# Performance work log

Hardware: AMD Instinct MI355X
Metric: run time of the kernel (lower is better)

Reference implementation:

```python
import jax, jax.numpy as jnp
import numpy as np

B, N = 4, 2048
EMB, HID = 64, 256
LENGTHSCALES = (0.5, 1.0, 2.0, 4.0)
H = len(LENGTHSCALES)
HEAD = HID // H  # 64, divides evenly
LAYERS = 4
IN_DIM = 3 + EMB + 3
EPS_LN = 1e-5


def _layer_norm(x, g, b):
    mu = jnp.mean(x, axis=-1, keepdims=True)
    var = jnp.mean((x - mu) ** 2, axis=-1, keepdims=True)
    return (x - mu) * jax.lax.rsqrt(var + EPS_LN) * g + b


def setup_inputs() -> dict:
    key = jax.random.key(0)
    ks = iter(jax.random.split(key, 32))
    p = lambda shape, s=0.02: jax.random.normal(next(ks), shape, jnp.float32) * s
    inp = {
        "latent_vars": jax.random.normal(next(ks), (B, N, 3), jnp.float32),
        "x_coords": jax.random.normal(next(ks), (B, N, 3), jnp.float32),
        "atom_embeddings": jax.random.normal(next(ks), (B, N, EMB), jnp.float32),
        # input MLP
        "in_W": p((IN_DIM, HID)), "in_b": jnp.zeros((HID,), jnp.float32),
        # per-layer kernel attention: per-head value projections + output projection
        "val_W": p((LAYERS, H, HID, HEAD)), "val_b": jnp.zeros((LAYERS, H, HEAD), jnp.float32),
        "attn_W": p((LAYERS, H * HEAD, HID)), "attn_b": jnp.zeros((LAYERS, HID), jnp.float32),
        # layer norms
        "ln1_g": jnp.ones((LAYERS, HID), jnp.float32), "ln1_b": jnp.zeros((LAYERS, HID), jnp.float32),
        "ln2_g": jnp.ones((LAYERS, HID), jnp.float32), "ln2_b": jnp.zeros((LAYERS, HID), jnp.float32),
        # FFN (hidden -> 2*hidden -> hidden)
        "ffn_W1": p((LAYERS, HID, 2 * HID)), "ffn_b1": jnp.zeros((LAYERS, 2 * HID), jnp.float32),
        "ffn_W2": p((LAYERS, 2 * HID, HID)), "ffn_b2": jnp.zeros((LAYERS, HID), jnp.float32),
        # output MLP
        "out_W1": p((HID, HID)), "out_b1": jnp.zeros((HID,), jnp.float32),
        "out_W2": p((HID, 3)), "out_b2": jnp.zeros((3,), jnp.float32),
    }
    return inp


def _forward(latent_vars, x_coords, atom_embeddings, in_W, in_b, val_W, val_b,
             attn_W, attn_b, ln1_g, ln1_b, ln2_g, ln2_b,
             ffn_W1, ffn_b1, ffn_W2, ffn_b2, out_W1, out_b1, out_W2, out_b2):
    # input MLP
    x = jnp.concatenate([x_coords, atom_embeddings, latent_vars], axis=-1)  # [B,N,70]
    feats = jax.nn.relu(x @ in_W + in_b)  # [B,N,HID]

    # RBF attention weights depend only on coords + fixed lengthscales -> compute once
    diff = x_coords[:, :, None, :] - x_coords[:, None, :, :]  # [B,N,N,3]
    d2 = jnp.sum(diff * diff, axis=-1)  # [B,N,N]
    ls2 = jnp.asarray(LENGTHSCALES, jnp.float32) ** 2  # [H]
    A = jnp.exp(-d2[None, :, :, :] / ls2[:, None, None, None])  # [H,B,N,N]
    A = A / (jnp.sum(A, axis=-1, keepdims=True) + 1e-8)

    for l in range(LAYERS):
        V = jnp.einsum('bnf,hfd->bnhd', feats, val_W[l]) + val_b[l]  # [B,N,H,HEAD]
        att = jnp.einsum('hbij,bjhd->bihd', A, V)  # [B,N,H,HEAD]
        att = att.reshape(att.shape[0], att.shape[1], H * HEAD) @ attn_W[l] + attn_b[l]
        feats = _layer_norm(feats + att, ln1_g[l], ln1_b[l])
        h = jax.nn.relu(feats @ ffn_W1[l] + ffn_b1[l]) @ ffn_W2[l] + ffn_b2[l]
        feats = _layer_norm(feats + h, ln2_g[l], ln2_b[l])

    return jax.nn.relu(feats @ out_W1 + out_b1) @ out_W2 + out_b2  # [B,N,3]


def reference(latent_vars, x_coords, atom_embeddings, in_W, in_b, val_W, val_b,
              attn_W, attn_b, ln1_g, ln1_b, ln2_g, ln2_b,
              ffn_W1, ffn_b1, ffn_W2, ffn_b2, out_W1, out_b1, out_W2, out_b2):
    return _forward(latent_vars, x_coords, atom_embeddings, in_W, in_b, val_W, val_b,
                    attn_W, attn_b, ln1_g, ln1_b, ln2_g, ln2_b,
                    ffn_W1, ffn_b1, ffn_W2, ffn_b2, out_W1, out_b1, out_W2, out_b2)
```

## Files before the change

kernel.cpp:

```cpp
#include <hip/hip_runtime.h>

#define B_ 4
#define N_ 2048
#define R_ (B_ * N_)
#define HID_ 256
#define EMB_ 64
#define IN_DIM_ 70
#define H_ 4
#define HEAD_ 64
#define FFN_ 512
#define LAYERS_ 4

typedef __attribute__((ext_vector_type(8))) short short8;
typedef __attribute__((ext_vector_type(4))) float f32x4;
typedef unsigned short ushort;

static __device__ __forceinline__ ushort f2bf(float f) {
    unsigned u = __builtin_bit_cast(unsigned, f);
    u += 0x7fffu + ((u >> 16) & 1u);
    return (ushort)(u >> 16);
}
static __device__ __forceinline__ float bf2f(ushort u) {
    unsigned x = ((unsigned)u) << 16;
    return __builtin_bit_cast(float, x);
}

#define GLOAD_LDS16(g, l)                                              \
    __builtin_amdgcn_global_load_lds(                                  \
        (const __attribute__((address_space(1))) void*)(g),            \
        (__attribute__((address_space(3))) void*)(l), 16, 0, 0)

#define MFMA16(a, b, c) __builtin_amdgcn_mfma_f32_16x16x32_bf16(a, b, c, 0, 0, 0)

__global__ __launch_bounds__(256) void pack_weights(const float* __restrict__ valW,
                                                    const float* __restrict__ attnW,
                                                    const float* __restrict__ ffnW1,
                                                    const float* __restrict__ ffnW2,
                                                    const float* __restrict__ outW1,
                                                    ushort* __restrict__ wp) {
    int idx = blockIdx.x * 256 + threadIdx.x;
    float v;
    if (idx < 262144) {
        int l = idx >> 16, c = (idx >> 8) & 255, k = idx & 255;
        v = valW[((l * 4 + (c >> 6)) * 256 + k) * 64 + (c & 63)];
    } else if (idx < 524288) {
        int i2 = idx - 262144;
        int l = i2 >> 16, c = (i2 >> 8) & 255, k = i2 & 255;
        v = attnW[l * 65536 + k * 256 + c];
    } else if (idx < 1048576) {
        int i2 = idx - 524288;
        int l = i2 >> 17, c = (i2 >> 8) & 511, k = i2 & 255;
        v = ffnW1[l * 131072 + k * 512 + c];
    } else if (idx < 1572864) {
        int i2 = idx - 1048576;
        int l = i2 >> 17, c = (i2 >> 9) & 255, k = i2 & 511;
        v = ffnW2[l * 131072 + k * 256 + c];
    } else {
        int i2 = idx - 1572864;
        int c = i2 >> 8, k = i2 & 255;
        v = outW1[k * 256 + c];
    }
    wp[idx] = f2bf(v);
}

__global__ __launch_bounds__(256) void input_mlp(const float* __restrict__ xc,
                                                 const float* __restrict__ emb,
                                                 const float* __restrict__ lat,
                                                 const float* __restrict__ W,
                                                 const float* __restrict__ b,
                                                 float* __restrict__ feats,
                                                 ushort* __restrict__ featsb) {
    __shared__ float xr[8][IN_DIM_ + 2];
    int t = threadIdx.x;
    int row0 = blockIdx.x * 8;
    for (int idx = t; idx < 8 * IN_DIM_; idx += 256) {
        int r = idx / IN_DIM_, f = idx % IN_DIM_;
        int rr = row0 + r;
        float v;
        if (f < 3)       v = xc[rr * 3 + f];
        else if (f < 67) v = emb[rr * EMB_ + (f - 3)];
        else             v = lat[rr * 3 + (f - 67)];
        xr[r][f] = v;
    }
    __syncthreads();
    float acc[8] = {0.f, 0.f, 0.f, 0.f, 0.f, 0.f, 0.f, 0.f};
    for (int f = 0; f < IN_DIM_; ++f) {
        float w = W[f * HID_ + t];
#pragma unroll
        for (int r = 0; r < 8; ++r) acc[r] += xr[r][f] * w;
    }
    float bb = b[t];
#pragma unroll
    for (int r = 0; r < 8; ++r) {
        float v = fmaxf(acc[r] + bb, 0.f);
        feats[(row0 + r) * HID_ + t] = v;
        featsb[(row0 + r) * HID_ + t] = f2bf(v);
    }
}

__global__ __launch_bounds__(256) void ebuild(const float* __restrict__ xc,
                                              ushort* __restrict__ E) {
    __shared__ float4 civ[64];
    __shared__ float4 cjv[512];
    int t = threadIdx.x;
    int jb = blockIdx.x;
    int ibl = blockIdx.y;
    int b = blockIdx.z;
    const float* xb = xc + (size_t)b * N_ * 3;
    if (t < 64) {
        const float* p = &xb[(ibl * 64 + t) * 3];
        float x = p[0], y = p[1], z = p[2];
        civ[t] = make_float4(x, y, z, x * x + y * y + z * z);
    }
#pragma unroll
    for (int s = 0; s < 2; ++s) {
        int j = s * 256 + t;
        const float* p = &xb[(jb * 512 + j) * 3];
        float x = p[0], y = p[1], z = p[2];
        cjv[j] = make_float4(x, y, z, x * x + y * y + z * z);
    }
    __syncthreads();
    int lane = t & 63, ig = t >> 6;
    float4 cj[8];
#pragma unroll
    for (int e = 0; e < 8; ++e) cj[e] = cjv[lane * 8 + e];
    const float ch0 = -4.f * 1.44269504088896f;
    ushort* Ebase = E + ((size_t)b * 2048 + ibl * 64) * 2048 + (size_t)jb * 512 + lane * 8;

    for (int r = 0; r < 16; ++r) {
        int i = ig * 16 + r;
        float4 ci = civ[i];
        float d[8];
#pragma unroll
        for (int e = 0; e < 8; ++e)
            d[e] = (ci.w + cj[e].w) -
                   2.f * (ci.x * cj[e].x + ci.y * cj[e].y + ci.z * cj[e].z);
        float ch = ch0;
#pragma unroll
        for (int h = 0; h < 4; ++h) {
            float ex[8];
#pragma unroll
            for (int e = 0; e < 8; ++e) ex[e] = exp2f(d[e] * ch);
            union { unsigned u[4]; uint4 v; } pk;
#pragma unroll
            for (int q = 0; q < 4; ++q)
                asm("v_cvt_pk_bf16_f32 %0, %1, %2"
                    : "=v"(pk.u[q]) : "v"(ex[2 * q]), "v"(ex[2 * q + 1]));
            *(uint4*)(Ebase + (size_t)h * 4 * 2048 * 2048 + (size_t)i * 2048) = pk.v;
            ch *= 0.25f;
        }
    }
}

__global__ __launch_bounds__(256, 1) void pv_gemm(const ushort* __restrict__ E,
                                                  const ushort* __restrict__ Vt,
                                                  ushort* __restrict__ attb) {
    __shared__ __align__(16) char lds[98304];
    int t = threadIdx.x;
    int l = t & 63, w = t >> 6;
    int lr = l & 15, g = l >> 4;

    int f = blockIdx.x;
    int xcd = f & 7, s = f >> 3;
    int combo = xcd * 2 + (s >> 4);
    int ib = s & 15;
    int b = combo & 3, h = combo >> 2;
    int i_base = ib * 128;
    int hc = h * 64;

    const ushort* Eb = E + (size_t)(h * 4 + b) * 2048 * 2048;

    const ushort* srcA[4];
    const ushort* srcB[2];
#pragma unroll
    for (int q = 0; q < 4; ++q) {
        int slotq = q * 256 + t;
        int arw = slotq >> 3, sl = slotq & 7;
        srcA[q] = Eb + (size_t)(i_base + arw) * 2048 + ((sl ^ (arw & 7)) << 3);
    }
#pragma unroll
    for (int q = 0; q < 2; ++q) {
        int slotq = q * 256 + t;
        int crw = slotq >> 3, sl = slotq & 7;
        srcB[q] = Vt + (size_t)(b * 256 + hc + crw) * 2048 + ((sl ^ (crw & 7)) << 3);
    }
    auto STAGE = [&](int c) {
        char* base = lds + (c & 3) * 24576;
#pragma unroll
        for (int q = 0; q < 4; ++q)
            GLOAD_LDS16(srcA[q] + c * 64, base + (q * 256 + t) * 16);
#pragma unroll
        for (int q = 0; q < 2; ++q)
            GLOAD_LDS16(srcB[q] + c * 64, base + 16384 + (q * 256 + t) * 16);
    };

    f32x4 acc[2][4] = {};
    f32x4 accd[2] = {};
    short8 ones = {0x3F80, 0x3F80, 0x3F80, 0x3F80, 0x3F80, 0x3F80, 0x3F80, 0x3F80};

    int sw_a = (lr & 7) << 4;
    int aoff0 = (w * 32 + lr) * 128;
    int aoff1 = (w * 32 + 16 + lr) * 128;

    auto COMPUTE = [&](int c) {
        const char* As = lds + (c & 3) * 24576;
        const char* Bs = As + 16384;
        short8 a00 = *(const short8*)(As + aoff0 + ((g * 16) ^ sw_a));
        short8 a01 = *(const short8*)(As + aoff0 + ((64 + g * 16) ^ sw_a));
        short8 a10 = *(const short8*)(As + aoff1 + ((g * 16) ^ sw_a));
        short8 a11 = *(const short8*)(As + aoff1 + ((64 + g * 16) ^ sw_a));
        accd[0] = MFMA16(a00, ones, accd[0]);
        accd[0] = MFMA16(a01, ones, accd[0]);
        accd[1] = MFMA16(a10, ones, accd[1]);
        accd[1] = MFMA16(a11, ones, accd[1]);
#pragma unroll
        for (int n = 0; n < 4; ++n) {
            int cc = n * 16 + lr;
            const char* cb = Bs + cc * 128;
            int sw = (cc & 7) << 4;
            short8 b0 = *(const short8*)(cb + ((g * 16) ^ sw));
            short8 b1 = *(const short8*)(cb + ((64 + g * 16) ^ sw));
            acc[0][n] = MFMA16(a00, b0, acc[0][n]);
            acc[0][n] = MFMA16(a01, b1, acc[0][n]);
            acc[1][n] = MFMA16(a10, b0, acc[1][n]);
            acc[1][n] = MFMA16(a11, b1, acc[1][n]);
        }
    };

    STAGE(0);
    STAGE(1);
    STAGE(2);

    for (int c = 0; c < 30; ++c) {
        asm volatile("s_waitcnt vmcnt(12)" ::: "memory");
        __builtin_amdgcn_s_barrier();
        __builtin_amdgcn_sched_barrier(0);
        if (c < 29) STAGE(c + 3);
        COMPUTE(c);
    }
    asm volatile("s_waitcnt vmcnt(6)" ::: "memory");
    __builtin_amdgcn_s_barrier();
    __builtin_amdgcn_sched_barrier(0);
    COMPUTE(30);
    asm volatile("s_waitcnt vmcnt(0)" ::: "memory");
    __builtin_amdgcn_s_barrier();
    __builtin_amdgcn_sched_barrier(0);
    COMPUTE(31);

#pragma unroll
    for (int m = 0; m < 2; ++m) {
#pragma unroll
        for (int r = 0; r < 4; ++r) {
            float invd = 1.f / (accd[m][r] + 1e-8f);
            int row = i_base + w * 32 + m * 16 + g * 4 + r;
            size_t rb = ((size_t)b * N_ + row) * 256 + hc + lr;
#pragma unroll
            for (int n = 0; n < 4; ++n)
                attb[rb + n * 16] = f2bf(acc[m][n][r] * invd);
        }
    }
}

template <int MODE>
__global__ __launch_bounds__(256) void gemmM(const ushort* __restrict__ A,
                                             const ushort* __restrict__ Bt,
                                             const float* __restrict__ bias,
                                             const float* __restrict__ resid,
                                             const float* __restrict__ lng,
                                             ushort* __restrict__ outb,
                                             float* __restrict__ outf) {
    __shared__ __align__(16) char lds[69632];
    int t = threadIdx.x;
    int l = t & 63, w = t >> 6;
    int lr = l & 15, g = l >> 4;
    int row0 = blockIdx.x * 16;
    f32x4 acc[4] = {};

    const ushort* srcA = A + (size_t)(row0 + (t >> 3)) * 256 + (((t & 7) ^ ((t >> 3) & 7)) << 3);
    const ushort* srcB[8];
#pragma unroll
    for (int q = 0; q < 8; ++q) {
        int cl = q * 32 + (t >> 3);
        srcB[q] = Bt + (size_t)cl * 256 + (((t & 7) ^ (cl & 7)) << 3);
    }
    auto STAGE = [&](int buf) {
        if (t < 128) GLOAD_LDS16(srcA, lds + buf * 2048 + t * 16);
#pragma unroll
        for (int q = 0; q < 8; ++q)
            GLOAD_LDS16(srcB[q], lds + 4096 + buf * 32768 + q * 4096 + t * 16);
        srcA += 64;
#pragma unroll
        for (int q = 0; q < 8; ++q) srcB[q] += 64;
    };

    int sw_a = (lr & 7) << 4;
    int aoff = lr * 128;

    STAGE(0);
#pragma unroll
    for (int c = 0; c < 4; ++c) {
        __syncthreads();
        if (c + 1 < 4) STAGE((c + 1) & 1);
        const char* As = lds + (c & 1) * 2048;
        const char* Ws = lds + 4096 + (c & 1) * 32768;

        short8 a0 = *(const short8*)(As + aoff + ((g * 16) ^ sw_a));
        short8 a1 = *(const short8*)(As + aoff + ((64 + g * 16) ^ sw_a));
#pragma unroll
        for (int n = 0; n < 4; ++n) {
            int cc = w * 64 + n * 16 + lr;
            const char* cb = Ws + cc * 128;
            int sw = (cc & 7) << 4;
            short8 b0 = *(const short8*)(cb + ((g * 16) ^ sw));
            short8 b1 = *(const short8*)(cb + ((64 + g * 16) ^ sw));
            acc[n] = MFMA16(a0, b0, acc[n]);
            acc[n] = MFMA16(a1, b1, acc[n]);
        }
    }
    __syncthreads();

    if constexpr (MODE == 3) {
        ushort(*Ts)[24] = (ushort(*)[24])lds;
#pragma unroll
        for (int n = 0; n < 4; ++n) {
            int c = w * 64 + n * 16 + lr;
            float bi = bias[c];
#pragma unroll
            for (int r = 0; r < 4; ++r)
                Ts[c][g * 4 + r] = f2bf(acc[n][r] + bi);
        }
        __syncthreads();
        {
            int c = t;
            int b = row0 >> 11;
            int n0 = row0 & 2047;
            ushort* dst = outb + ((size_t)(b * 256 + c)) * 2048 + n0;
            *(uint4*)dst = *(uint4*)&Ts[c][0];
            *(uint4*)(dst + 8) = *(uint4*)&Ts[c][8];
        }
    } else {
        const float* W2 = resid;
        const float* b2 = lng;
        ushort(*Ts)[264] = (ushort(*)[264])lds;
#pragma unroll
        for (int n = 0; n < 4; ++n) {
            int c = w * 64 + n * 16 + lr;
            float bi = bias[c];
#pragma unroll
            for (int r = 0; r < 4; ++r)
                Ts[g * 4 + r][c] = f2bf(fmaxf(acc[n][r] + bi, 0.f));
        }
        __syncthreads();
        int row = t >> 4, sg = t & 15;
        float p0 = 0.f, p1 = 0.f, p2 = 0.f;
#pragma unroll
        for (int e = 0; e < 16; ++e) {
            float x = bf2f(Ts[row][sg * 16 + e]);
            const float* wr = &W2[(sg * 16 + e) * 3];
            p0 += x * wr[0];
            p1 += x * wr[1];
            p2 += x * wr[2];
        }
#pragma unroll
        for (int off = 1; off < 16; off <<= 1) {
            p0 += __shfl_xor(p0, off, 64);
            p1 += __shfl_xor(p1, off, 64);
            p2 += __shfl_xor(p2, off, 64);
        }
        if (sg == 0) {
            int gr = row0 + row;
            outf[gr * 3 + 0] = p0 + b2[0];
            outf[gr * 3 + 1] = p1 + b2[1];
            outf[gr * 3 + 2] = p2 + b2[2];
        }
    }
}

__global__ __launch_bounds__(512) void gemm_layer(
        const ushort* __restrict__ attb,
        const ushort* __restrict__ Wat, const float* __restrict__ pb,
        float* __restrict__ feats,
        const float* __restrict__ ln1g, const float* __restrict__ ln1b,
        const ushort* __restrict__ W1t, const float* __restrict__ b1,
        const ushort* __restrict__ W2t, const float* __restrict__ b2,
        const float* __restrict__ ln2g, const float* __restrict__ ln2b,
        ushort* __restrict__ featsb,
        const ushort* __restrict__ WvN, const float* __restrict__ vbN,
        ushort* __restrict__ Vt) {
    __shared__ __align__(16) char lds[122880];
    char* Aa = lds;
    char* Asp = lds + 8192;
    char* Wsp = lds + 24576;
    char* hidp = lds + 90112;

    int t = threadIdx.x;
    int l = t & 63, w = t >> 6;
    int cg = w & 3, mh = w >> 2;
    int lr = l & 15, g = l >> 4;
    int row0 = blockIdx.x * 32;
    int arow = mh * 16 + lr;
    int sw_a = (lr & 7) << 4;
    int trow = t >> 3, slot = t & 7;

    uint4 wA0, wA1, wA2, wA3;
    uint4 wB0, wB1, wB2, wB3;
    auto WLOADA = [&](const ushort* Wb, int stride, int colbase, int c) {
        const ushort* base = Wb + c * 64;
#pragma unroll
        for (int q = 0; q < 4; ++q) {
            int cl = colbase + q * 64 + trow;
            uint4 v = *(const uint4*)(base + (size_t)cl * stride + ((slot ^ (cl & 7)) << 3));
            if (q == 0) wA0 = v; else if (q == 1) wA1 = v;
            else if (q == 2) wA2 = v; else wA3 = v;
        }
    };
    auto WLOADB = [&](const ushort* Wb, int stride, int colbase, int c) {
        const ushort* base = Wb + c * 64;
#pragma unroll
        for (int q = 0; q < 4; ++q) {
            int cl = colbase + q * 64 + trow;
            uint4 v = *(const uint4*)(base + (size_t)cl * stride + ((slot ^ (cl & 7)) << 3));
            if (q == 0) wB0 = v; else if (q == 1) wB1 = v;
            else if (q == 2) wB2 = v; else wB3 = v;
        }
    };
    auto WSTOREA = [&]() {
        *(uint4*)(Wsp + 0 * 8192 + t * 16) = wA0;
        *(uint4*)(Wsp + 1 * 8192 + t * 16) = wA1;
        *(uint4*)(Wsp + 2 * 8192 + t * 16) = wA2;
        *(uint4*)(Wsp + 3 * 8192 + t * 16) = wA3;
    };
    auto WSTOREB = [&]() {
        char* base = Wsp + 32768;
        *(uint4*)(base + 0 * 8192 + t * 16) = wB0;
        *(uint4*)(base + 1 * 8192 + t * 16) = wB1;
        *(uint4*)(base + 2 * 8192 + t * 16) = wB2;
        *(uint4*)(base + 3 * 8192 + t * 16) = wB3;
    };

    const ushort* srcA = attb + (size_t)(row0 + trow) * 256 + ((slot ^ (trow & 7)) << 3);
    auto STAGEA = [&](int buf, int c) {
        if (t < 256) GLOAD_LDS16(srcA + c * 64, Aa + buf * 4096 + t * 16);
    };

    f32x4 acc0[4] = {};
    STAGEA(0, 0);
    WLOADA(Wat, 256, 0, 0);
#pragma unroll
    for (int c = 0; c < 4; ++c) {
        __syncthreads();
        WSTOREA();
        __syncthreads();
        if (c < 3) { WLOADA(Wat, 256, 0, c + 1); STAGEA((c + 1) & 1, c + 1); }
        else WLOADA(W1t, 256, 0, 0);

        const char* As = Aa + (c & 1) * 4096;
        short8 a0 = *(const short8*)(As + arow * 128 + ((g * 16) ^ sw_a));
        short8 a1 = *(const short8*)(As + arow * 128 + ((64 + g * 16) ^ sw_a));
#pragma unroll
        for (int n = 0; n < 4; ++n) {
            int cc = cg * 64 + n * 16 + lr;
            const char* cb = Wsp + cc * 128;
            int sw = (cc & 7) << 4;
            short8 b0 = *(const short8*)(cb + ((g * 16) ^ sw));
            short8 b1 = *(const short8*)(cb + ((64 + g * 16) ^ sw));
            acc0[n] = MFMA16(a0, b0, acc0[n]);
            acc0[n] = MFMA16(a1, b1, acc0[n]);
        }
    }
    __syncthreads();

    float* red1 = (float*)lds;
    float* red2 = (float*)(lds + 512);
    float x1v[4][4];
    {
        float s1[4] = {0.f, 0.f, 0.f, 0.f}, s2[4] = {0.f, 0.f, 0.f, 0.f};
#pragma unroll
        for (int n = 0; n < 4; ++n) {
            int c = cg * 64 + n * 16 + lr;
            float bi = pb[c];
#pragma unroll
            for (int r = 0; r < 4; ++r) {
                int row = row0 + mh * 16 + g * 4 + r;
                float v = acc0[n][r] + bi + feats[(size_t)row * 256 + c];
                x1v[n][r] = v;
                s1[r] += v;
                s2[r] += v * v;
            }
        }
#pragma unroll
        for (int off = 1; off < 16; off <<= 1) {
#pragma unroll
            for (int r = 0; r < 4; ++r) {
                s1[r] += __shfl_xor(s1[r], off, 64);
                s2[r] += __shfl_xor(s2[r], off, 64);
            }
        }
        if (lr == 0) {
#pragma unroll
            for (int r = 0; r < 4; ++r) {
                red1[(mh * 16 + g * 4 + r) * 4 + cg] = s1[r];
                red2[(mh * 16 + g * 4 + r) * 4 + cg] = s2[r];
            }
        }
        __syncthreads();
#pragma unroll
        for (int n = 0; n < 4; ++n) {
            int c = cg * 64 + n * 16 + lr;
            float gg = ln1g[c], bb = ln1b[c];
#pragma unroll
            for (int r = 0; r < 4; ++r) {
                int rr = mh * 16 + g * 4 + r;
                float m1 = red1[rr * 4] + red1[rr * 4 + 1] + red1[rr * 4 + 2] + red1[rr * 4 + 3];
                float m2 = red2[rr * 4] + red2[rr * 4 + 1] + red2[rr * 4 + 2] + red2[rr * 4 + 3];
                float mu = m1 * (1.f / 256.f);
                float var = m2 * (1.f / 256.f) - mu * mu;
                float rstd = rsqrtf(var + 1e-5f);
                float o = (x1v[n][r] - mu) * rstd * gg + bb;
                x1v[n][r] = o;
                *(ushort*)(Asp + rr * 512 + ((2 * c) ^ ((rr & 7) << 4))) = f2bf(o);
            }
        }
    }

    WSTOREA();
    WLOADB(W1t, 256, 0, 1);
    asm volatile("s_waitcnt lgkmcnt(0)" ::: "memory");
    __builtin_amdgcn_sched_barrier(0);
    __builtin_amdgcn_s_barrier();

    f32x4 acc1[4] = {}, acc1b[4] = {}, acc2[4] = {};
#pragma unroll
    for (int u = 0; u < 16; ++u) {
        const char* WB = Wsp + (u & 1) * 32768;
        short8 a0, a1;
        if (u < 8) {
            int c = u & 3;
            a0 = *(const short8*)(Asp + arow * 512 + ((c * 128 + g * 16) ^ sw_a));
            a1 = *(const short8*)(Asp + arow * 512 + ((c * 128 + 64 + g * 16) ^ sw_a));
        } else {
            int c = u - 8;
            a0 = *(const short8*)(hidp + arow * 1024 + ((c * 128 + g * 16) ^ sw_a));
            a1 = *(const short8*)(hidp + arow * 1024 + ((c * 128 + 64 + g * 16) ^ sw_a));
        }
#pragma unroll
        for (int n = 0; n < 4; ++n) {
            int cc = cg * 64 + n * 16 + lr;
            const char* cb = WB + cc * 128;
            int sw = (cc & 7) << 4;
            short8 b0 = *(const short8*)(cb + ((g * 16) ^ sw));
            short8 b1 = *(const short8*)(cb + ((64 + g * 16) ^ sw));
            if (u < 4)      { acc1[n] = MFMA16(a0, b0, acc1[n]);  acc1[n] = MFMA16(a1, b1, acc1[n]); }
            else if (u < 8) { acc1b[n] = MFMA16(a0, b0, acc1b[n]); acc1b[n] = MFMA16(a1, b1, acc1b[n]); }
            else            { acc2[n] = MFMA16(a0, b0, acc2[n]);  acc2[n] = MFMA16(a1, b1, acc2[n]); }
        }
        if (u == 3) {
#pragma unroll
            for (int n = 0; n < 4; ++n) {
                int cf = cg * 64 + n * 16 + lr;
                float bi = b1[cf];
#pragma unroll
                for (int r = 0; r < 4; ++r) {
                    int rw = mh * 16 + g * 4 + r;
                    float v = fmaxf(acc1[n][r] + bi, 0.f);
                    *(ushort*)(hidp + rw * 1024 + ((cf * 2) ^ ((rw & 7) << 4))) = f2bf(v);
                }
            }
        }
        if (u == 7) {
#pragma unroll
            for (int n = 0; n < 4; ++n) {
                int cf = 256 + cg * 64 + n * 16 + lr;
                float bi = b1[cf];
#pragma unroll
                for (int r = 0; r < 4; ++r) {
                    int rw = mh * 16 + g * 4 + r;
                    float v = fmaxf(acc1b[n][r] + bi, 0.f);
                    *(ushort*)(hidp + rw * 1024 + ((cf * 2) ^ ((rw & 7) << 4))) = f2bf(v);
                }
            }
        }
        {
            int k = u + 2;
            bool issued = true;
            if (k < 4)       { if (u & 1) WLOADB(W1t, 256, 0, k);       else WLOADA(W1t, 256, 0, k); }
            else if (k < 8)  { if (u & 1) WLOADB(W1t, 256, 256, k - 4); else WLOADA(W1t, 256, 256, k - 4); }
            else if (k < 16) { if (u & 1) WLOADB(W2t, 512, 0, k - 8);   else WLOADA(W2t, 512, 0, k - 8); }
            else if (WvN)    { if (u & 1) WLOADB(WvN, 256, 0, k - 16);  else WLOADA(WvN, 256, 0, k - 16); }
            else issued = false;
            if (issued) asm volatile("s_waitcnt vmcnt(4)" ::: "memory");
            else        asm volatile("s_waitcnt vmcnt(0)" ::: "memory");
            __builtin_amdgcn_sched_barrier(0);
            if (u < 15 || WvN) { if ((u + 1) & 1) WSTOREB(); else WSTOREA(); }
            asm volatile("s_waitcnt lgkmcnt(0)" ::: "memory");
            __builtin_amdgcn_sched_barrier(0);
            __builtin_amdgcn_s_barrier();
        }
    }

#pragma unroll
    for (int n = 0; n < 4; ++n) {
        int c = cg * 64 + n * 16 + lr;
        float bi = b2[c];
#pragma unroll
        for (int r = 0; r < 4; ++r)
            acc2[n][r] = acc2[n][r] + bi + x1v[n][r];
    }
    {
        float* red1b = (float*)lds;
        float* red2b = (float*)(lds + 512);
        float s1[4] = {0.f, 0.f, 0.f, 0.f}, s2[4] = {0.f, 0.f, 0.f, 0.f};
#pragma unroll
        for (int n = 0; n < 4; ++n)
#pragma unroll
            for (int r = 0; r < 4; ++r) {
                s1[r] += acc2[n][r];
                s2[r] += acc2[n][r] * acc2[n][r];
            }
#pragma unroll
        for (int off = 1; off < 16; off <<= 1) {
#pragma unroll
            for (int r = 0; r < 4; ++r) {
                s1[r] += __shfl_xor(s1[r], off, 64);
                s2[r] += __shfl_xor(s2[r], off, 64);
            }
        }
        if (lr == 0) {
#pragma unroll
            for (int r = 0; r < 4; ++r) {
                red1b[(mh * 16 + g * 4 + r) * 4 + cg] = s1[r];
                red2b[(mh * 16 + g * 4 + r) * 4 + cg] = s2[r];
            }
        }
        __syncthreads();
#pragma unroll
        for (int n = 0; n < 4; ++n) {
            int c = cg * 64 + n * 16 + lr;
            float gg = ln2g[c], bb = ln2b[c];
#pragma unroll
            for (int r = 0; r < 4; ++r) {
                int rr = mh * 16 + g * 4 + r;
                float m1 = red1b[rr * 4] + red1b[rr * 4 + 1] + red1b[rr * 4 + 2] + red1b[rr * 4 + 3];
                float m2 = red2b[rr * 4] + red2b[rr * 4 + 1] + red2b[rr * 4 + 2] + red2b[rr * 4 + 3];
                float mu = m1 * (1.f / 256.f);
                float var = m2 * (1.f / 256.f) - mu * mu;
                float rstd = rsqrtf(var + 1e-5f);
                int row = row0 + rr;
                float o = (acc2[n][r] - mu) * rstd * gg + bb;
                feats[(size_t)row * 256 + c] = o;
                ushort ob = f2bf(o);
                featsb[(size_t)row * 256 + c] = ob;
                *(ushort*)(Asp + rr * 512 + ((2 * c) ^ ((rr & 7) << 4))) = ob;
            }
        }
    }
    __syncthreads();

    if (WvN) {
        f32x4 acc3[4] = {};
#pragma unroll
        for (int u3 = 0; u3 < 4; ++u3) {
            const char* WB = Wsp + (u3 & 1) * 32768;
            short8 a0 = *(const short8*)(Asp + arow * 512 + ((u3 * 128 + g * 16) ^ sw_a));
            short8 a1 = *(const short8*)(Asp + arow * 512 + ((u3 * 128 + 64 + g * 16) ^ sw_a));
#pragma unroll
            for (int n = 0; n < 4; ++n) {
                int cc = cg * 64 + n * 16 + lr;
                const char* cb = WB + cc * 128;
                int sw = (cc & 7) << 4;
                short8 b0 = *(const short8*)(cb + ((g * 16) ^ sw));
                short8 b1 = *(const short8*)(cb + ((64 + g * 16) ^ sw));
                acc3[n] = MFMA16(a0, b0, acc3[n]);
                acc3[n] = MFMA16(a1, b1, acc3[n]);
            }
            if (u3 < 3) {
                if (u3 < 2) {
                    if (u3 & 1) WLOADB(WvN, 256, 0, u3 + 2);
                    else        WLOADA(WvN, 256, 0, u3 + 2);
                    asm volatile("s_waitcnt vmcnt(4)" ::: "memory");
                } else {
                    asm volatile("s_waitcnt vmcnt(0)" ::: "memory");
                }
                __builtin_amdgcn_sched_barrier(0);
                if ((u3 + 1) & 1) WSTOREB(); else WSTOREA();
                asm volatile("s_waitcnt lgkmcnt(0)" ::: "memory");
                __builtin_amdgcn_sched_barrier(0);
                __builtin_amdgcn_s_barrier();
            }
        }
        __syncthreads();
        ushort(*Ts)[40] = (ushort(*)[40])hidp;
#pragma unroll
        for (int n = 0; n < 4; ++n) {
            int c = cg * 64 + n * 16 + lr;
            float bi = vbN[c];
#pragma unroll
            for (int r = 0; r < 4; ++r)
                Ts[c][mh * 16 + g * 4 + r] = f2bf(acc3[n][r] + bi);
        }
        __syncthreads();
        if (t < 256) {
            int c = t;
            int b = row0 >> 11;
            int n0 = row0 & 2047;
            ushort* dst = Vt + ((size_t)(b * 256 + c)) * 2048 + n0;
            *(uint4*)dst = *(uint4*)&Ts[c][0];
            *(uint4*)(dst + 8) = *(uint4*)&Ts[c][8];
            *(uint4*)(dst + 16) = *(uint4*)&Ts[c][16];
            *(uint4*)(dst + 24) = *(uint4*)&Ts[c][24];
        }
    }
}

extern "C" void kernel_launch(void* const* d_in, const int* in_sizes, int n_in,
                              void* d_out, int out_size, void* d_ws, size_t ws_size,
                              hipStream_t stream) {
    const float* lat    = (const float*)d_in[0];
    const float* xc     = (const float*)d_in[1];
    const float* emb    = (const float*)d_in[2];
    const float* in_W   = (const float*)d_in[3];
    const float* in_b   = (const float*)d_in[4];
    const float* val_W  = (const float*)d_in[5];
    const float* val_b  = (const float*)d_in[6];
    const float* attn_W = (const float*)d_in[7];
    const float* attn_b = (const float*)d_in[8];
    const float* ln1_g  = (const float*)d_in[9];
    const float* ln1_b  = (const float*)d_in[10];
    const float* ln2_g  = (const float*)d_in[11];
    const float* ln2_b  = (const float*)d_in[12];
    const float* ffn_W1 = (const float*)d_in[13];
    const float* ffn_b1 = (const float*)d_in[14];
    const float* ffn_W2 = (const float*)d_in[15];
    const float* ffn_b2 = (const float*)d_in[16];
    const float* out_W1 = (const float*)d_in[17];
    const float* out_b1 = (const float*)d_in[18];
    const float* out_W2 = (const float*)d_in[19];
    const float* out_b2 = (const float*)d_in[20];

    char* W = (char*)d_ws;
    float*  feats  = (float*)W;
    ushort* featsb = (ushort*)(W + (8u << 20));
    ushort* attb   = (ushort*)(W + (12u << 20));
    ushort* Vt     = (ushort*)(W + (16u << 20));
    ushort* wp     = (ushort*)(W + (20u << 20));
    ushort* E      = (ushort*)(W + (24u << 20));
    ushort* Wvt  = wp;
    ushort* Wat  = wp + 262144;
    ushort* W1t  = wp + 524288;
    ushort* W2t  = wp + 1048576;
    ushort* Wo1t = wp + 1572864;

    pack_weights<<<6400, 256, 0, stream>>>(val_W, attn_W, ffn_W1, ffn_W2, out_W1, wp);
    input_mlp<<<R_ / 8, 256, 0, stream>>>(xc, emb, lat, in_W, in_b, feats, featsb);
    ebuild<<<dim3(4, 32, B_), 256, 0, stream>>>(xc, E);

    gemmM<3><<<R_ / 16, 256, 0, stream>>>(
        featsb, Wvt, val_b, nullptr, nullptr, Vt, nullptr);

    for (int l = 0; l < LAYERS_; ++l) {
        pv_gemm<<<256, 256, 0, stream>>>(E, Vt, attb);
        const ushort* WvN = (l + 1 < LAYERS_) ? (Wvt + (l + 1) * 65536) : nullptr;
        const float* vbN = val_b + ((l + 1 < LAYERS_) ? (l + 1) * 256 : 0);
        gemm_layer<<<R_ / 32, 512, 0, stream>>>(
            attb, Wat + l * 65536, attn_b + l * 256,
            feats, ln1_g + l * 256, ln1_b + l * 256,
            W1t + l * 131072, ffn_b1 + l * 512,
            W2t + l * 131072, ffn_b2 + l * 256,
            ln2_g + l * 256, ln2_b + l * 256,
            featsb, WvN, vbN, Vt);
    }

    gemmM<4><<<R_ / 16, 256, 0, stream>>>(
        featsb, Wo1t, out_b1, out_W2, out_b2, nullptr, (float*)d_out);
}
```

Before: 244.9 us.

## Store RBF attention matrix and values in FP8, use FP8 MFMA in PV GEMM

The unnormalized RBF kernel matrix E and the transposed value matrix Vt are now stored as FP8 instead of BF16, and the PV GEMM uses FP8 MFMA instructions, with the row-sum computed against an FP8 ones vector. This halves the bytes streamed from the large E tensor on each of the four layers and halves LDS use, which drops the one-block-per-CU launch bound. The LDS swizzle and staging counts are reworked for the 64-byte rows. The cost is reduced precision in the attention weights and values, which risks accuracy tolerance failures.

```diff
diff --git a/kernel.cpp b/kernel.cpp
--- a/kernel.cpp
+++ b/kernel.cpp
@@ -14,6 +14,8 @@
 typedef __attribute__((ext_vector_type(8))) short short8;
 typedef __attribute__((ext_vector_type(4))) float f32x4;
 typedef unsigned short ushort;
+typedef unsigned char uchar;
+typedef unsigned long ulong_t;
 
 static __device__ __forceinline__ ushort f2bf(float f) {
     unsigned u = __builtin_bit_cast(unsigned, f);
@@ -31,6 +33,7 @@
         (__attribute__((address_space(3))) void*)(l), 16, 0, 0)
 
 #define MFMA16(a, b, c) __builtin_amdgcn_mfma_f32_16x16x32_bf16(a, b, c, 0, 0, 0)
+#define MFMA8(a, b, c) __builtin_amdgcn_mfma_f32_16x16x32_fp8_fp8(a, b, c, 0, 0, 0)
 
 __global__ __launch_bounds__(256) void pack_weights(const float* __restrict__ valW,
                                                     const float* __restrict__ attnW,
@@ -99,7 +102,7 @@
 }
 
 __global__ __launch_bounds__(256) void ebuild(const float* __restrict__ xc,
-                                              ushort* __restrict__ E) {
+                                              uchar* __restrict__ E) {
     __shared__ float4 civ[64];
     __shared__ float4 cjv[512];
     int t = threadIdx.x;
@@ -125,7 +128,7 @@
 #pragma unroll
     for (int e = 0; e < 8; ++e) cj[e] = cjv[lane * 8 + e];
     const float ch0 = -4.f * 1.44269504088896f;
-    ushort* Ebase = E + ((size_t)b * 2048 + ibl * 64) * 2048 + (size_t)jb * 512 + lane * 8;
+    uchar* Ebase = E + ((size_t)b * 2048 + ibl * 64) * 2048 + (size_t)jb * 512 + lane * 8;
 
     for (int r = 0; r < 16; ++r) {
         int i = ig * 16 + r;
@@ -141,21 +144,24 @@
             float ex[8];
 #pragma unroll
             for (int e = 0; e < 8; ++e) ex[e] = exp2f(d[e] * ch);
-            union { unsigned u[4]; uint4 v; } pk;
-#pragma unroll
-            for (int q = 0; q < 4; ++q)
-                asm("v_cvt_pk_bf16_f32 %0, %1, %2"
-                    : "=v"(pk.u[q]) : "v"(ex[2 * q]), "v"(ex[2 * q + 1]));
-            *(uint4*)(Ebase + (size_t)h * 4 * 2048 * 2048 + (size_t)i * 2048) = pk.v;
+            int lo = 0, hi = 0;
+            lo = __builtin_amdgcn_cvt_pk_fp8_f32(ex[0], ex[1], lo, false);
+            lo = __builtin_amdgcn_cvt_pk_fp8_f32(ex[2], ex[3], lo, true);
+            hi = __builtin_amdgcn_cvt_pk_fp8_f32(ex[4], ex[5], hi, false);
+            hi = __builtin_amdgcn_cvt_pk_fp8_f32(ex[6], ex[7], hi, true);
+            uint2 val;
+            val.x = (unsigned)lo;
+            val.y = (unsigned)hi;
+            *(uint2*)(Ebase + (size_t)h * 4 * 2048 * 2048 + (size_t)i * 2048) = val;
             ch *= 0.25f;
         }
     }
 }
 
-__global__ __launch_bounds__(256, 1) void pv_gemm(const ushort* __restrict__ E,
-                                                  const ushort* __restrict__ Vt,
-                                                  ushort* __restrict__ attb) {
-    __shared__ __align__(16) char lds[98304];
+__global__ __launch_bounds__(256) void pv_gemm(const uchar* __restrict__ E,
+                                               const uchar* __restrict__ Vt,
+                                               ushort* __restrict__ attb) {
+    __shared__ __align__(16) char lds[49152];
     int t = threadIdx.x;
     int l = t & 63, w = t >> 6;
     int lr = l & 15, g = l >> 4;
@@ -168,62 +174,53 @@
     int i_base = ib * 128;
     int hc = h * 64;
 
-    const ushort* Eb = E + (size_t)(h * 4 + b) * 2048 * 2048;
-
-    const ushort* srcA[4];
-    const ushort* srcB[2];
-#pragma unroll
-    for (int q = 0; q < 4; ++q) {
-        int slotq = q * 256 + t;
-        int arw = slotq >> 3, sl = slotq & 7;
-        srcA[q] = Eb + (size_t)(i_base + arw) * 2048 + ((sl ^ (arw & 7)) << 3);
-    }
+    const uchar* Eb = E + (size_t)(h * 4 + b) * 2048 * 2048;
+    const uchar* VtB = Vt + (size_t)(b * 256 + hc) * 2048;
+
+    const uchar* srcA[2];
 #pragma unroll
     for (int q = 0; q < 2; ++q) {
         int slotq = q * 256 + t;
-        int crw = slotq >> 3, sl = slotq & 7;
-        srcB[q] = Vt + (size_t)(b * 256 + hc + crw) * 2048 + ((sl ^ (crw & 7)) << 3);
+        int row = slotq >> 2, p = slotq & 3;
+        srcA[q] = Eb + (size_t)(i_base + row) * 2048 + ((p ^ ((row >> 1) & 3)) << 4);
+    }
+    const uchar* srcV;
+    {
+        int col = t >> 2, p = t & 3;
+        srcV = VtB + (size_t)col * 2048 + ((p ^ ((col >> 1) & 3)) << 4);
     }
     auto STAGE = [&](int c) {
-        char* base = lds + (c & 3) * 24576;
-#pragma unroll
-        for (int q = 0; q < 4; ++q)
+        char* base = lds + (c & 3) * 12288;
+#pragma unroll
+        for (int q = 0; q < 2; ++q)
             GLOAD_LDS16(srcA[q] + c * 64, base + (q * 256 + t) * 16);
-#pragma unroll
-        for (int q = 0; q < 2; ++q)
-            GLOAD_LDS16(srcB[q] + c * 64, base + 16384 + (q * 256 + t) * 16);
+        GLOAD_LDS16(srcV + c * 64, base + 8192 + t * 16);
     };
 
     f32x4 acc[2][4] = {};
     f32x4 accd[2] = {};
-    short8 ones = {0x3F80, 0x3F80, 0x3F80, 0x3F80, 0x3F80, 0x3F80, 0x3F80, 0x3F80};
-
-    int sw_a = (lr & 7) << 4;
-    int aoff0 = (w * 32 + lr) * 128;
-    int aoff1 = (w * 32 + 16 + lr) * 128;
+    const long ones8 = 0x3838383838383838L;
+
+    int r0 = w * 32 + lr;
+    int r1 = r0 + 16;
 
     auto COMPUTE = [&](int c) {
-        const char* As = lds + (c & 3) * 24576;
-        const char* Bs = As + 16384;
-        short8 a00 = *(const short8*)(As + aoff0 + ((g * 16) ^ sw_a));
-        short8 a01 = *(const short8*)(As + aoff0 + ((64 + g * 16) ^ sw_a));
-        short8 a10 = *(const short8*)(As + aoff1 + ((g * 16) ^ sw_a));
-        short8 a11 = *(const short8*)(As + aoff1 + ((64 + g * 16) ^ sw_a));
-        accd[0] = MFMA16(a00, ones, accd[0]);
-        accd[0] = MFMA16(a01, ones, accd[0]);
-        accd[1] = MFMA16(a10, ones, accd[1]);
-        accd[1] = MFMA16(a11, ones, accd[1]);
-#pragma unroll
-        for (int n = 0; n < 4; ++n) {
-            int cc = n * 16 + lr;
-            const char* cb = Bs + cc * 128;
-            int sw = (cc & 7) << 4;
-            short8 b0 = *(const short8*)(cb + ((g * 16) ^ sw));
-            short8 b1 = *(const short8*)(cb + ((64 + g * 16) ^ sw));
-            acc[0][n] = MFMA16(a00, b0, acc[0][n]);
-            acc[0][n] = MFMA16(a01, b1, acc[0][n]);
-            acc[1][n] = MFMA16(a10, b0, acc[1][n]);
-            acc[1][n] = MFMA16(a11, b1, acc[1][n]);
+        const char* As = lds + (c & 3) * 12288;
+        const char* Vs = As + 8192;
+#pragma unroll
+        for (int kk = 0; kk < 2; ++kk) {
+            int off = kk * 32 + g * 8;
+            long a0 = *(const long*)(As + r0 * 64 + (off ^ (((r0 >> 1) & 3) << 4)));
+            long a1 = *(const long*)(As + r1 * 64 + (off ^ (((r1 >> 1) & 3) << 4)));
+            accd[0] = MFMA8(a0, ones8, accd[0]);
+            accd[1] = MFMA8(a1, ones8, accd[1]);
+#pragma unroll
+            for (int n = 0; n < 4; ++n) {
+                int col = n * 16 + lr;
+                long bv = *(const long*)(Vs + col * 64 + (off ^ (((col >> 1) & 3) << 4)));
+                acc[0][n] = MFMA8(a0, bv, acc[0][n]);
+                acc[1][n] = MFMA8(a1, bv, acc[1][n]);
+            }
         }
     };
 
@@ -232,13 +229,13 @@
     STAGE(2);
 
     for (int c = 0; c < 30; ++c) {
-        asm volatile("s_waitcnt vmcnt(12)" ::: "memory");
+        asm volatile("s_waitcnt vmcnt(6)" ::: "memory");
         __builtin_amdgcn_s_barrier();
         __builtin_amdgcn_sched_barrier(0);
         if (c < 29) STAGE(c + 3);
         COMPUTE(c);
     }
-    asm volatile("s_waitcnt vmcnt(6)" ::: "memory");
+    asm volatile("s_waitcnt vmcnt(3)" ::: "memory");
     __builtin_amdgcn_s_barrier();
     __builtin_amdgcn_sched_barrier(0);
     COMPUTE(30);
@@ -267,7 +264,7 @@
                                              const float* __restrict__ bias,
                                              const float* __restrict__ resid,
                                              const float* __restrict__ lng,
-                                             ushort* __restrict__ outb,
+                                             uchar* __restrict__ outb,
                                              float* __restrict__ outf) {
     __shared__ __align__(16) char lds[69632];
     int t = threadIdx.x;
@@ -320,28 +317,27 @@
     __syncthreads();
 
     if constexpr (MODE == 3) {
-        ushort(*Ts)[24] = (ushort(*)[24])lds;
+        uchar* Ts = (uchar*)(lds + 8192);
 #pragma unroll
         for (int n = 0; n < 4; ++n) {
             int c = w * 64 + n * 16 + lr;
             float bi = bias[c];
-#pragma unroll
-            for (int r = 0; r < 4; ++r)
-                Ts[c][g * 4 + r] = f2bf(acc[n][r] + bi);
+            int u = 0;
+            u = __builtin_amdgcn_cvt_pk_fp8_f32(acc[n][0] + bi, acc[n][1] + bi, u, false);
+            u = __builtin_amdgcn_cvt_pk_fp8_f32(acc[n][2] + bi, acc[n][3] + bi, u, true);
+            *(int*)(Ts + c * 16 + g * 4) = u;
         }
         __syncthreads();
         {
             int c = t;
             int b = row0 >> 11;
             int n0 = row0 & 2047;
-            ushort* dst = outb + ((size_t)(b * 256 + c)) * 2048 + n0;
-            *(uint4*)dst = *(uint4*)&Ts[c][0];
-            *(uint4*)(dst + 8) = *(uint4*)&Ts[c][8];
+            *(uint4*)(outb + ((size_t)(b * 256 + c)) * 2048 + n0) = *(uint4*)(Ts + c * 16);
         }
     } else {
         const float* W2 = resid;
         const float* b2 = lng;
-        ushort(*Ts)[264] = (ushort(*)[264])lds;
+        ushort(*Ts)[264] = (ushort(*)[264])(lds + 8192);
 #pragma unroll
         for (int n = 0; n < 4; ++n) {
             int c = w * 64 + n * 16 + lr;
@@ -386,7 +382,7 @@
         const float* __restrict__ ln2g, const float* __restrict__ ln2b,
         ushort* __restrict__ featsb,
         const ushort* __restrict__ WvN, const float* __restrict__ vbN,
-        ushort* __restrict__ Vt) {
+        uchar* __restrict__ Vt) {
     __shared__ __align__(16) char lds[122880];
     char* Aa = lds;
     char* Asp = lds + 8192;
@@ -689,25 +685,24 @@
             }
         }
         __syncthreads();
-        ushort(*Ts)[40] = (ushort(*)[40])hidp;
+        uchar* Ts = (uchar*)hidp;
 #pragma unroll
         for (int n = 0; n < 4; ++n) {
             int c = cg * 64 + n * 16 + lr;
             float bi = vbN[c];
-#pragma unroll
-            for (int r = 0; r < 4; ++r)
-                Ts[c][mh * 16 + g * 4 + r] = f2bf(acc3[n][r] + bi);
+            int u = 0;
+            u = __builtin_amdgcn_cvt_pk_fp8_f32(acc3[n][0] + bi, acc3[n][1] + bi, u, false);
+            u = __builtin_amdgcn_cvt_pk_fp8_f32(acc3[n][2] + bi, acc3[n][3] + bi, u, true);
+            *(int*)(Ts + c * 32 + mh * 16 + g * 4) = u;
         }
         __syncthreads();
         if (t < 256) {
             int c = t;
             int b = row0 >> 11;
             int n0 = row0 & 2047;
-            ushort* dst = Vt + ((size_t)(b * 256 + c)) * 2048 + n0;
-            *(uint4*)dst = *(uint4*)&Ts[c][0];
-            *(uint4*)(dst + 8) = *(uint4*)&Ts[c][8];
-            *(uint4*)(dst + 16) = *(uint4*)&Ts[c][16];
-            *(uint4*)(dst + 24) = *(uint4*)&Ts[c][24];
+            uchar* dst = Vt + ((size_t)(b * 256 + c)) * 2048 + n0;
+            *(uint4*)dst = *(uint4*)(Ts + c * 32);
+            *(uint4*)(dst + 16) = *(uint4*)(Ts + c * 32 + 16);
         }
     }
 }
@@ -741,9 +736,9 @@
     float*  feats  = (float*)W;
     ushort* featsb = (ushort*)(W + (8u << 20));
     ushort* attb   = (ushort*)(W + (12u << 20));
-    ushort* Vt     = (ushort*)(W + (16u << 20));
+    uchar*  Vt8    = (uchar*)(W + (16u << 20));
     ushort* wp     = (ushort*)(W + (20u << 20));
-    ushort* E      = (ushort*)(W + (24u << 20));
+    uchar*  E8     = (uchar*)(W + (24u << 20));
     ushort* Wvt  = wp;
     ushort* Wat  = wp + 262144;
     ushort* W1t  = wp + 524288;
@@ -752,13 +747,13 @@
 
     pack_weights<<<6400, 256, 0, stream>>>(val_W, attn_W, ffn_W1, ffn_W2, out_W1, wp);
     input_mlp<<<R_ / 8, 256, 0, stream>>>(xc, emb, lat, in_W, in_b, feats, featsb);
-    ebuild<<<dim3(4, 32, B_), 256, 0, stream>>>(xc, E);
+    ebuild<<<dim3(4, 32, B_), 256, 0, stream>>>(xc, E8);
 
     gemmM<3><<<R_ / 16, 256, 0, stream>>>(
-        featsb, Wvt, val_b, nullptr, nullptr, Vt, nullptr);
+        featsb, Wvt, val_b, nullptr, nullptr, Vt8, nullptr);
 
     for (int l = 0; l < LAYERS_; ++l) {
-        pv_gemm<<<256, 256, 0, stream>>>(E, Vt, attb);
+        pv_gemm<<<256, 256, 0, stream>>>(E8, Vt8, attb);
         const ushort* WvN = (l + 1 < LAYERS_) ? (Wvt + (l + 1) * 65536) : nullptr;
         const float* vbN = val_b + ((l + 1 < LAYERS_) ? (l + 1) * 256 : 0);
         gemm_layer<<<R_ / 32, 512, 0, stream>>>(
@@ -767,7 +762,7 @@
             W1t + l * 131072, ffn_b1 + l * 512,
             W2t + l * 131072, ffn_b2 + l * 256,
             ln2_g + l * 256, ln2_b + l * 256,
-            featsb, WvN, vbN, Vt);
+            featsb, WvN, vbN, Vt8);
     }
 
     gemmM<4><<<R_ / 16, 256, 0, stream>>>(
```

New measurement: 219.0 us. 10.6% less time.
